# Optimization experiments

Measured on AMD Instinct MI355X. Metric: run time of the kernel, lower is better.

Reference implementation:

```python
import jax, jax.numpy as jnp
import numpy as np
from jax import lax

EPS = 1e-5

# sign binarization with straight-through-estimator gradient (identity),
# matching the .data-swap trick in BinarizeConv2d/BinarizeLinear.
@jax.custom_vjp
def ste_sign(x):
    return jnp.sign(x)

def _ste_fwd(x):
    return jnp.sign(x), None

def _ste_bwd(_, g):
    return (g,)

ste_sign.defvjp(_ste_fwd, _ste_bwd)


def conv3x3(x, w):
    # weight is binarized inside the layer; padding=1, stride=1, no bias
    return lax.conv_general_dilated(
        x, ste_sign(w), window_strides=(1, 1), padding=((1, 1), (1, 1)),
        dimension_numbers=('NCHW', 'OIHW', 'NCHW'))


def mp2(x):
    return lax.reduce_window(x, -jnp.inf, lax.max, (1, 1, 2, 2), (1, 1, 2, 2), 'VALID')


def bn2d(x, gamma, beta):
    # training-mode BatchNorm2d: batch statistics over (N, H, W)
    mu = jnp.mean(x, axis=(0, 2, 3), keepdims=True)
    var = jnp.var(x, axis=(0, 2, 3), keepdims=True)
    xn = (x - mu) * lax.rsqrt(var + EPS)
    return xn * gamma[None, :, None, None] + beta[None, :, None, None]


def bn1d(x, gamma=None, beta=None):
    mu = jnp.mean(x, axis=0, keepdims=True)
    var = jnp.var(x, axis=0, keepdims=True)
    xn = (x - mu) * lax.rsqrt(var + EPS)
    if gamma is None:
        return xn
    return xn * gamma[None, :] + beta[None, :]


def hardtanh(x):
    return jnp.clip(x, -1.0, 1.0)


def setup_inputs() -> dict:
    key = jax.random.key(0)
    ks = jax.random.split(key, 16)
    def w(k, shape):
        return jax.random.normal(k, shape, jnp.float32) * 0.1
    d = {'x': jax.random.normal(ks[0], (512, 3, 32, 32), jnp.float32)}
    convs = [(64, 3), (64, 64), (128, 64), (128, 128), (256, 128), (256, 256)]
    for i, (co, ci) in enumerate(convs):
        d[f'w{i+1}'] = w(ks[1 + i], (co, ci, 3, 3))
        d[f'g{i+1}'] = jnp.ones((co,), jnp.float32)
        d[f'b{i+1}'] = jnp.zeros((co,), jnp.float32)
    d['wf1'] = w(ks[7], (512, 256 * 4 * 4))
    d['gf1'] = jnp.ones((512,), jnp.float32)
    d['bf1'] = jnp.zeros((512,), jnp.float32)
    d['wf2'] = w(ks[8], (512, 512))
    d['gf2'] = jnp.ones((512,), jnp.float32)
    d['bf2'] = jnp.zeros((512,), jnp.float32)
    d['wf3'] = w(ks[9], (10, 512))
    return d


def reference(x, w1, g1, b1, w2, g2, b2, w3, g3, b3, w4, g4, b4,
              w5, g5, b5, w6, g6, b6, wf1, gf1, bf1, wf2, gf2, bf2, wf3):
    # block 1: first conv sees raw 3-channel input (not binarized)
    h = hardtanh(bn2d(conv3x3(x, w1), g1, b1))
    h = hardtanh(bn2d(mp2(conv3x3(ste_sign(h), w2)), g2, b2))
    # block 2
    h = hardtanh(bn2d(conv3x3(ste_sign(h), w3), g3, b3))
    h = hardtanh(bn2d(mp2(conv3x3(ste_sign(h), w4)), g4, b4))
    # block 3
    h = hardtanh(bn2d(conv3x3(ste_sign(h), w5), g5, b5))
    h = hardtanh(bn2d(mp2(conv3x3(ste_sign(h), w6)), g6, b6))
    # classifier (all linear inputs binarized: feature dim != 784)
    h = h.reshape(-1, 256 * 4 * 4)
    h = hardtanh(bn1d(ste_sign(h) @ ste_sign(wf1).T, gf1, bf1))
    h = hardtanh(bn1d(ste_sign(h) @ ste_sign(wf2).T, gf2, bf2))
    h = bn1d(ste_sign(h) @ ste_sign(wf3).T)  # affine=False
    return jax.nn.log_softmax(h, axis=-1)
```

## Files before the change

kernel.cpp:

```cpp
#include <hip/hip_runtime.h>
#include <stdint.h>
#include <math.h>


typedef unsigned long long u64;

__device__ __forceinline__ void flag_and_wave(u64* flag, u64 nz) {
    nz &= __shfl_xor(nz, 1);
    nz &= __shfl_xor(nz, 2);
    nz &= __shfl_xor(nz, 4);
    nz &= __shfl_xor(nz, 8);
    nz &= __shfl_xor(nz, 16);
    nz &= __shfl_xor(nz, 32);
    if ((threadIdx.x & 63) == 0) atomicAnd(flag, nz);
}

__global__ void kflag_init(u64* __restrict__ f) {
    int i = threadIdx.x;
    if (i < 16) f[i] = ~0ull;
}

__global__ void kw1t(const float* __restrict__ w1, float* __restrict__ wt) {
    int i = blockIdx.x * 64 + threadIdx.x;
    if (i >= 64 * 27) return;
    int co = i / 27, k = i % 27;
    float v = w1[i];
    wt[k * 64 + co] = (v > 0.f) ? 1.f : ((v < 0.f) ? -1.f : 0.f);
}

__global__ __launch_bounds__(256) void k1_conv_allv2(const float* __restrict__ x,
                                                     const float* __restrict__ wt,
                                                     float* __restrict__ out) {
    int gid = blockIdx.x * 256 + threadIdx.x;
    int n = gid >> 8, hw0 = (gid & 255) * 4;
    int cbase = blockIdx.y * 32;
    int y = hw0 >> 5, x0 = hw0 & 31;
    const float* ip = x + (size_t)n * 3 * 1024;
    for (int cc = 0; cc < 32; cc += 16) {
        int c0 = cbase + cc;
        float4 a[16];
#pragma unroll
        for (int c = 0; c < 16; ++c) a[c] = make_float4(0.f, 0.f, 0.f, 0.f);
        for (int ky = 0; ky < 3; ++ky) {
            int yy = y + ky - 1;
            bool rowok = (unsigned)yy < 32u;
            float win[3][6];
#pragma unroll
            for (int ci = 0; ci < 3; ++ci)
#pragma unroll
                for (int j = 0; j < 6; ++j) {
                    int ccx = x0 - 1 + j;
                    bool ok = rowok && ((unsigned)ccx < 32u);
                    win[ci][j] = ok ? ip[ci * 1024 + yy * 32 + ccx] : 0.f;
                }
#pragma unroll
            for (int kx = 0; kx < 3; ++kx)
#pragma unroll
                for (int ci = 0; ci < 3; ++ci) {
                    const float* wrow = wt + (ci * 9 + ky * 3 + kx) * 64 + c0;
                    float s0 = win[ci][kx], s1 = win[ci][kx + 1];
                    float s2 = win[ci][kx + 2], s3 = win[ci][kx + 3];
#pragma unroll
                    for (int c = 0; c < 16; ++c) {
                        float wv = wrow[c];
                        a[c].x = fmaf(wv, s0, a[c].x);
                        a[c].y = fmaf(wv, s1, a[c].y);
                        a[c].z = fmaf(wv, s2, a[c].z);
                        a[c].w = fmaf(wv, s3, a[c].w);
                    }
                }
        }
#pragma unroll
        for (int c = 0; c < 16; ++c)
            *(float4*)(out + ((size_t)n * 64 + c0 + c) * 1024 + hw0) = a[c];
    }
}

__global__ void k1_statsA(const float* __restrict__ v, double* __restrict__ Sp,
                          double* __restrict__ S2p, int N) {
    int c = blockIdx.x;
    int slot = blockIdx.y * 64 + threadIdx.x;
    double s = 0.0, s2 = 0.0;
    int K = N * 4;
    const float* vp = v + (size_t)c * 1024 + slot;
    int k0 = 0;
    for (; k0 + 32 <= K; k0 += 32) {
        const float* p0 = vp + (size_t)(k0 >> 2) * 65536;
        float buf[32];
#pragma unroll
        for (int j = 0; j < 32; ++j)
            buf[j] = p0[(size_t)(j >> 2) * 65536 + (j & 3) * 256];
#pragma unroll
        for (int j = 0; j < 32; ++j) {
            double t = (double)buf[j];
            s += t; s2 += t * t;
        }
    }
    for (; k0 < K; ++k0) {
        int m = slot + k0 * 256;
        double t = (double)v[((size_t)(m >> 10) * 64 + c) * 1024 + (m & 1023)];
        s += t; s2 += t * t;
    }
// ... 192 lines not shown
                          const float* __restrict__ w6, const float* __restrict__ wf1,
                          const float* __restrict__ wf2, const float* __restrict__ wf3,
                          u64* wb2B, u64* wb2Z, u64* wb3B, u64* wb3Z,
                          u64* wb4B, u64* wb4Z, u64* wb5B, u64* wb5Z,
                          u64* wb6B, u64* wb6Z, u64* wf1B, u64* wf1Z,
                          u64* wf2B, u64* wf2Z, u64* wf3B, u64* wf3Z,
                          u64* flags) {
    int b = blockIdx.x, t = threadIdx.x;
    if      (b <   3) pack_wconv_body(w2, wb2B, wb2Z,  64,  64, &flags[0], b * 256 + t);
    else if (b <   8) pack_wconv_body(w3, wb3B, wb3Z,  64, 128, &flags[1], (b - 3) * 256 + t);
    else if (b <  17) pack_wconv_body(w4, wb4B, wb4Z, 128, 128, &flags[2], (b - 8) * 256 + t);
    else if (b <  35) pack_wconv_body(w5, wb5B, wb5Z, 128, 256, &flags[3], (b - 17) * 256 + t);
    else if (b <  71) pack_wconv_body(w6, wb6B, wb6Z, 256, 256, &flags[4], (b - 35) * 256 + t);
    else if (b < 199) pack_wlinT_body(wf1, wf1B, wf1Z, 4096, 512, &flags[5], (b - 71) * 256 + t);
    else if (b < 215) pack_wlinT_body(wf2, wf2B, wf2Z,  512, 512, &flags[6], (b - 199) * 256 + t);
    else              pack_wlinT_body(wf3, wf3B, wf3Z,  512,  10, &flags[7], (b - 215) * 256 + t);
}

template <int WRD, int CB>
__device__ __forceinline__ void conv_slow(const u64* __restrict__ ib, const u64* __restrict__ iz,
                                          const u64* __restrict__ wbp, const u64* __restrict__ wzp,
                                          int H, int Wi, int y, int x, int* acc) {
#pragma unroll
    for (int c = 0; c < CB; ++c) acc[c] = 0;
    for (int ky = 0; ky < 3; ++ky) {
        int yy = y + ky - 1;
        if ((unsigned)yy >= (unsigned)H) continue;
        for (int kx = 0; kx < 3; ++kx) {
            int xc = x + kx - 1;
            if ((unsigned)xc >= (unsigned)Wi) continue;
            int p = yy * Wi + xc, t = ky * 3 + kx;
            u64 xb[WRD], xz[WRD];
#pragma unroll
            for (int w = 0; w < WRD; ++w) {
                xb[w] = ib[(size_t)p * WRD + w];
                xz[w] = iz[(size_t)p * WRD + w];
            }
#pragma unroll
            for (int c = 0; c < CB; ++c) {
#pragma unroll
                for (int w = 0; w < WRD; ++w) {
                    u64 e = xz[w] & wzp[(c * 9 + t) * WRD + w];
                    acc[c] += __popcll(e) - 2 * __popcll((xb[w] ^ wbp[(c * 9 + t) * WRD + w]) & e);
                }
            }
        }
    }
}

template <int WRD, int CB>
__device__ __forceinline__ void conv_fast(const u64* __restrict__ ib,
                                          const u64* __restrict__ wbp,
                                          int H, int Wi, int y, int x, int* acc) {
    int a2[CB];
#pragma unroll
    for (int c = 0; c < CB; ++c) a2[c] = 0;
    int T = 0;
    for (int ky = 0; ky < 3; ++ky) {
        int yy = y + ky - 1;
        if ((unsigned)yy >= (unsigned)H) continue;
        for (int kx = 0; kx < 3; ++kx) {
            int xc = x + kx - 1;
            if ((unsigned)xc >= (unsigned)Wi) continue;
            int p = yy * Wi + xc, t = ky * 3 + kx;
            ++T;
            u64 xb[WRD];
#pragma unroll
            for (int w = 0; w < WRD; ++w) xb[w] = ib[(size_t)p * WRD + w];
#pragma unroll
            for (int c = 0; c < CB; ++c)
#pragma unroll
                for (int w = 0; w < WRD; ++w)
                    a2[c] += __popcll(xb[w] ^ wbp[(c * 9 + t) * WRD + w]);
        }
    }
#pragma unroll
    for (int c = 0; c < CB; ++c) acc[c] = 64 * WRD * T - 2 * a2[c];
}

template <int WRD, int CB>
__global__ void kbconv2(const u64* __restrict__ B, const u64* __restrict__ NZ,
                        const u64* __restrict__ WB, const u64* __restrict__ WNZ,
                        int16_t* __restrict__ out, int Co, int H, int Wi,
                        const u64* __restrict__ wflag, const u64* __restrict__ aflag) {
    int hw = blockIdx.x * 64 + threadIdx.x;
    if (hw >= H * Wi) return;
    int co0 = blockIdx.y * CB, n = blockIdx.z;
    int y = hw / Wi, x = hw % Wi;
    const u64* ib = B  + (size_t)n * H * Wi * WRD;
    const u64* iz = NZ + (size_t)n * H * Wi * WRD;
    const u64* wbp = WB  + (size_t)co0 * 9 * WRD;
    const u64* wzp = WNZ + (size_t)co0 * 9 * WRD;
    bool fast = ((*wflag) & (*aflag)) == ~0ull;
    int acc[CB];
    if (fast) conv_fast<WRD, CB>(ib, wbp, H, Wi, y, x, acc);
    else      conv_slow<WRD, CB>(ib, iz, wbp, wzp, H, Wi, y, x, acc);
#pragma unroll
    for (int c = 0; c < CB; ++c)
        out[((size_t)n * Co + co0 + c) * H * Wi + hw] = (int16_t)acc[c];
}

template <int WRD, int CB>
__global__ void kbconv_pool2(const u64* __restrict__ B, const u64* __restrict__ NZ,
                             const u64* __restrict__ WB, const u64* __restrict__ WNZ,
                             int16_t* __restrict__ out, int Co, int H, int Wi,
                             const u64* __restrict__ wflag, const u64* __restrict__ aflag) {
    int Ho = H >> 1, Wo = Wi >> 1;
    int hw = blockIdx.x * 64 + threadIdx.x;
    if (hw >= Ho * Wo) return;
    int co0 = blockIdx.y * CB, n = blockIdx.z;
    int yo = hw / Wo, xo = hw % Wo;
    const u64* ib = B  + (size_t)n * H * Wi * WRD;
    const u64* iz = NZ + (size_t)n * H * Wi * WRD;
    const u64* wbp = WB  + (size_t)co0 * 9 * WRD;
    const u64* wzp = WNZ + (size_t)co0 * 9 * WRD;
    bool fast = ((*wflag) & (*aflag)) == ~0ull;
    int best[CB];
#pragma unroll
    for (int c = 0; c < CB; ++c) best[c] = -(1 << 30);
    if (fast) {
        for (int dy = 0; dy < 2; ++dy)
            for (int dx = 0; dx < 2; ++dx) {
                int acc[CB];
                conv_fast<WRD, CB>(ib, wbp, H, Wi, 2 * yo + dy, 2 * xo + dx, acc);
#pragma unroll
                for (int c = 0; c < CB; ++c) best[c] = acc[c] > best[c] ? acc[c] : best[c];
            }
    } else {
        for (int dy = 0; dy < 2; ++dy)
            for (int dx = 0; dx < 2; ++dx) {
                int acc[CB];
                conv_slow<WRD, CB>(ib, iz, wbp, wzp, H, Wi, 2 * yo + dy, 2 * xo + dx, acc);
#pragma unroll
                for (int c = 0; c < CB; ++c) best[c] = acc[c] > best[c] ? acc[c] : best[c];
            }
    }
#pragma unroll
    for (int c = 0; c < CB; ++c)
        out[((size_t)n * Co + co0 + c) * Ho * Wo + hw] = (int16_t)best[c];
}

template <int WRD, int CB>
__global__ void kbconv_pool2s(const u64* __restrict__ B, const u64* __restrict__ NZ,
                              const u64* __restrict__ WB, const u64* __restrict__ WNZ,
                              int16_t* __restrict__ out, int Co, int H, int Wi,
                              const u64* __restrict__ wflag, const u64* __restrict__ aflag) {
    int Ho = H >> 1, Wo = Wi >> 1;
    int t0 = threadIdx.x;
    int pix = t0 & 15, pos = t0 >> 4;
    int co0 = blockIdx.y * CB, n = blockIdx.z;
    int yo = pix / Wo, xo = pix % Wo;
    int y = 2 * yo + (pos >> 1), x = 2 * xo + (pos & 1);
    const u64* ib = B  + (size_t)n * H * Wi * WRD;
    const u64* iz = NZ + (size_t)n * H * Wi * WRD;
    const u64* wbp = WB  + (size_t)co0 * 9 * WRD;
    const u64* wzp = WNZ + (size_t)co0 * 9 * WRD;
    bool fast = ((*wflag) & (*aflag)) == ~0ull;
    int acc[CB];
    if (fast) conv_fast<WRD, CB>(ib, wbp, H, Wi, y, x, acc);
    else      conv_slow<WRD, CB>(ib, iz, wbp, wzp, H, Wi, y, x, acc);
#pragma unroll
    for (int c = 0; c < CB; ++c) {
        int v = acc[c];
        int v1 = __shfl_xor(v, 16); v = v1 > v ? v1 : v;
        int v2 = __shfl_xor(v, 32); v = v2 > v ? v2 : v;
        acc[c] = v;
    }
    if (pos == 0) {
#pragma unroll
        for (int c = 0; c < CB; ++c)
            out[((size_t)n * Co + co0 + c) * Ho * Wo + pix] = (int16_t)acc[c];
    }
}

__global__ void kaccum16(const int16_t* __restrict__ v, long long* __restrict__ Sp,
                         long long* __restrict__ S2p, int C, int HW, int M) {
    int c = blockIdx.x;
    long long s = 0, s2 = 0;
    int M8 = M >> 3;
    for (int g = blockIdx.y * 256 + threadIdx.x; g < M8; g += gridDim.y * 256) {
        int m0 = g * 8;
        const int16_t* p = v + ((size_t)(m0 / HW) * C + c) * HW + (m0 % HW);
        short4 a = *(const short4*)p;
        short4 b = *(const short4*)(p + 4);
        int v0 = a.x, v1 = a.y, v2 = a.z, v3 = a.w;
        int v4 = b.x, v5 = b.y, v6 = b.z, v7 = b.w;
        s  += v0 + v1 + v2 + v3 + v4 + v5 + v6 + v7;
        s2 += (long long)v0 * v0 + (long long)v1 * v1 + (long long)v2 * v2 + (long long)v3 * v3
            + (long long)v4 * v4 + (long long)v5 * v5 + (long long)v6 * v6 + (long long)v7 * v7;
    }
    __shared__ long long sh[256], sh2[256];
    sh[threadIdx.x] = s; sh2[threadIdx.x] = s2;
    __syncthreads();
    for (int o = 128; o > 0; o >>= 1) {
        if ((int)threadIdx.x < o) { sh[threadIdx.x] += sh[threadIdx.x + o]; sh2[threadIdx.x] += sh2[threadIdx.x + o]; }
        __syncthreads();
    }
    if (threadIdx.x == 0) {
        Sp[c * gridDim.y + blockIdx.y]  = sh[0];
        S2p[c * gridDim.y + blockIdx.y] = sh2[0];
    }
}

__global__ void ksp_conv2(const int16_t* __restrict__ v,
                          const long long* __restrict__ Sp, const long long* __restrict__ S2p,
                          int NB, const float* __restrict__ g, const float* __restrict__ b,
                          u64* __restrict__ B, u64* __restrict__ NZ, int C, int HW, int N,
                          int M, u64* __restrict__ aflag) {
    __shared__ double sMu[256], sA[256], sB[256];
    for (int c = threadIdx.x; c < C; c += 64) {
        long long s = 0, s2 = 0;
        for (int i = 0; i < NB; ++i) { s += Sp[c * NB + i]; s2 += S2p[c * NB + i]; }
        double mean = (double)s / M;
        double var  = (double)s2 / M - mean * mean;
        if (var < 0.0) var = 0.0;
        sMu[c] = mean;
        sA[c]  = (g ? (double)g[c] : 1.0) / sqrt(var + 1e-5);
        sB[c]  = b ? (double)b[c] : 0.0;
    }
    __syncthreads();
    int tid = blockIdx.x * 64 + threadIdx.x;
    int WRD = C >> 6;
    int HW4 = HW >> 2;
    int total = N * WRD * HW4;
    u64 nzall = ~0ull;
    if (tid < total) {
        int hw4 = tid % HW4;
        int wd  = (tid / HW4) % WRD;
        int n   = tid / (HW4 * WRD);
        const int16_t* vp = v + ((size_t)n * C + wd * 64) * HW + hw4 * 4;
        u64 b0 = 0, b1 = 0, b2 = 0, b3 = 0;
        u64 n0 = 0, n1 = 0, n2 = 0, n3 = 0;
        for (int j0 = 0; j0 < 64; j0 += 16) {
            short4 buf[16];
#pragma unroll
            for (int j = 0; j < 16; ++j)
                buf[j] = *(const short4*)(vp + (size_t)(j0 + j) * HW);
#pragma unroll
            for (int j = 0; j < 16; ++j) {
                int c = wd * 64 + j0 + j;
                double Mu = sMu[c], A = sA[c], Bb = sB[c];
                double t0 = ((double)buf[j].x - Mu) * A + Bb;
                double t1 = ((double)buf[j].y - Mu) * A + Bb;
                double t2 = ((double)buf[j].z - Mu) * A + Bb;
                double t3 = ((double)buf[j].w - Mu) * A + Bb;
                int sh = j0 + j;
                b0 |= (u64)(t0 > 0.0) << sh;  n0 |= (u64)(t0 != 0.0) << sh;
                b1 |= (u64)(t1 > 0.0) << sh;  n1 |= (u64)(t1 != 0.0) << sh;
                b2 |= (u64)(t2 > 0.0) << sh;  n2 |= (u64)(t2 != 0.0) << sh;
                b3 |= (u64)(t3 > 0.0) << sh;  n3 |= (u64)(t3 != 0.0) << sh;
            }
        }
        size_t o = ((size_t)n * HW + hw4 * 4) * WRD + wd;
        B[o] = b0;  B[o + WRD] = b1;  B[o + 2 * WRD] = b2;  B[o + 3 * WRD] = b3;
        NZ[o] = n0; NZ[o + WRD] = n1; NZ[o + 2 * WRD] = n2; NZ[o + 3 * WRD] = n3;
        nzall = n0 & n1 & n2 & n3;
    }
    flag_and_wave(aflag, nzall);
}

__global__ void ksp_flat2(const int16_t* __restrict__ v,
                          const long long* __restrict__ Sp, const long long* __restrict__ S2p,
                          int NB, const float* __restrict__ g, const float* __restrict__ b,
                          u64* __restrict__ B, u64* __restrict__ NZ, int M,
                          u64* __restrict__ aflag) {
    __shared__ double sMu[256], sA[256], sB[256];
    for (int c = threadIdx.x; c < 256; c += 64) {
        long long s = 0, s2 = 0;
        for (int i = 0; i < NB; ++i) { s += Sp[c * NB + i]; s2 += S2p[c * NB + i]; }
        double mean = (double)s / M;
        double var  = (double)s2 / M - mean * mean;
        if (var < 0.0) var = 0.0;
        sMu[c] = mean;
        sA[c]  = (g ? (double)g[c] : 1.0) / sqrt(var + 1e-5);
        sB[c]  = b ? (double)b[c] : 0.0;
    }
    __syncthreads();
    int wd = threadIdx.x;
    int n  = blockIdx.x;
    const int16_t* vp = v + (size_t)n * 4096 + wd * 64;
    int16_t buf[64];
#pragma unroll
    for (int j = 0; j < 64; ++j) buf[j] = vp[j];
    u64 b2 = 0, nz = 0;
#pragma unroll
    for (int j = 0; j < 64; ++j) {
        int k = wd * 64 + j;
        int c = k >> 4;
        double t = ((double)buf[j] - sMu[c]) * sA[c] + sB[c];
        b2 |= (u64)(t > 0.0) << j;
        nz |= (u64)(t != 0.0) << j;
    }
    B[(size_t)n * 64 + wd] = b2; NZ[(size_t)n * 64 + wd] = nz;
    flag_and_wave(aflag, nz);
}

__global__ void ksp_fc(const int* __restrict__ v, const double* __restrict__ mu,
                       const double* __restrict__ Ad, const double* __restrict__ Bd,
                       u64* __restrict__ B, u64* __restrict__ NZ, int C, int WRD, int N,
                       u64* __restrict__ aflag) {
    int tid = blockIdx.x * 64 + threadIdx.x;
    u64 nz = ~0ull;
    if (tid < N * WRD) {
        int n = tid / WRD, wd = tid % WRD;
        const int* vp = v + (size_t)n * C + wd * 64;
        int buf[64];
#pragma unroll
        for (int j = 0; j < 64; ++j) buf[j] = vp[j];
        u64 b = 0; nz = 0;
#pragma unroll
        for (int j = 0; j < 64; ++j) {
            int c = wd * 64 + j;
            double t = ((double)buf[j] - mu[c]) * Ad[c] + Bd[c];
            b  |= (u64)(t > 0.0) << j;
            nz |= (u64)(t != 0.0) << j;
        }
        B[(size_t)n * WRD + wd] = b; NZ[(size_t)n * WRD + wd] = nz;
    }
    flag_and_wave(aflag, nz);
}

__global__ void kbfc(const u64* __restrict__ aB, const u64* __restrict__ aNZ,
                     const u64* __restrict__ wBt, const u64* __restrict__ wZt,
                     int* __restrict__ out, int WRD, int O,
                     const u64* __restrict__ wflag, const u64* __restrict__ aflag) {
    int o = blockIdx.x * 64 + threadIdx.x;
    if (o >= O) return;
    int n = blockIdx.y;
    const u64* ab = aB  + (size_t)n * WRD;
    const u64* az = aNZ + (size_t)n * WRD;
    bool fast = ((*wflag) & (*aflag)) == ~0ull;
    int acc;
    if (fast) {
        int a2 = 0;
        for (int w = 0; w < WRD; w += 8) {
            u64 aw[8], ww[8];
#pragma unroll
            for (int j = 0; j < 8; ++j) {
                aw[j] = ab[w + j];
                ww[j] = wBt[(size_t)(w + j) * O + o];
            }
#pragma unroll
            for (int j = 0; j < 8; ++j) a2 += __popcll(aw[j] ^ ww[j]);
        }
        acc = 64 * WRD - 2 * a2;
    } else {
        acc = 0;
        for (int w = 0; w < WRD; ++w) {
            u64 wb = wBt[(size_t)w * O + o];
            u64 wz = wZt[(size_t)w * O + o];
            u64 e = az[w] & wz;
            acc += __popcll(e) - 2 * __popcll((ab[w] ^ wb) & e);
        }
    }
    out[(size_t)n * O + o] = acc;
}

__global__ void k3_stats(const int* __restrict__ v, int N, int C,
                         const float* __restrict__ g, const float* __restrict__ b,
                         double* __restrict__ mu, double* __restrict__ Ad,
                         double* __restrict__ Bd) {
    int c = blockIdx.x;
    __shared__ double sh[256], sh2[256];
    double s = 0.0, s2 = 0.0;
    for (int n = threadIdx.x; n < N; n += 256) {
        double t = (double)v[(size_t)n * C + c];
        s += t; s2 += t * t;
    }
    sh[threadIdx.x] = s; sh2[threadIdx.x] = s2;
    __syncthreads();
    for (int o = 128; o > 0; o >>= 1) {
        if ((int)threadIdx.x < o) { sh[threadIdx.x] += sh[threadIdx.x + o]; sh2[threadIdx.x] += sh2[threadIdx.x + o]; }
        __syncthreads();
    }
    if (threadIdx.x == 0) {
        double mean = sh[0] / N;
        double var  = sh2[0] / N - mean * mean;
        if (var < 0.0) var = 0.0;
        mu[c] = mean;
        Ad[c] = (g ? (double)g[c] : 1.0) / sqrt(var + 1e-5);
        Bd[c] = b ? (double)b[c] : 0.0;
    }
}

__global__ void k4_out(const int* __restrict__ v, const double* __restrict__ mu,
                       const double* __restrict__ Ad, float* __restrict__ out, int N) {
    int n = blockIdx.x * 256 + threadIdx.x;
    if (n >= N) return;
    double z[10];
    double mx = -1e300;
    for (int o = 0; o < 10; ++o) {
        z[o] = ((double)v[n * 10 + o] - mu[o]) * Ad[o];
        if (z[o] > mx) mx = z[o];
    }
    double s = 0.0;
    for (int o = 0; o < 10; ++o) s += exp(z[o] - mx);
    double l = mx + log(s);
    for (int o = 0; o < 10; ++o) out[n * 10 + o] = (float)(z[o] - l);
}

extern "C" void kernel_launch(void* const* d_in, const int* in_sizes, int n_in,
                              void* d_out, int out_size, void* d_ws, size_t ws_size,
                              hipStream_t stream) {
    const int N = in_sizes[0] / (3 * 32 * 32);

    const float* x   = (const float*)d_in[0];
    const float* w1  = (const float*)d_in[1];
    const float* g1  = (const float*)d_in[2];
    const float* b1  = (const float*)d_in[3];
    const float* w2  = (const float*)d_in[4];
    const float* g2  = (const float*)d_in[5];
    const float* b2  = (const float*)d_in[6];
    const float* w3  = (const float*)d_in[7];
    const float* g3  = (const float*)d_in[8];
    const float* b3  = (const float*)d_in[9];
    const float* w4  = (const float*)d_in[10];
    const float* g4  = (const float*)d_in[11];
    const float* b4  = (const float*)d_in[12];
    const float* w5  = (const float*)d_in[13];
    const float* g5  = (const float*)d_in[14];
    const float* b5  = (const float*)d_in[15];
    const float* w6  = (const float*)d_in[16];
    const float* g6  = (const float*)d_in[17];
    const float* b6  = (const float*)d_in[18];
    const float* wf1 = (const float*)d_in[19];
    const float* gf1 = (const float*)d_in[20];
    const float* bf1 = (const float*)d_in[21];
    const float* wf2 = (const float*)d_in[22];
    const float* gf2 = (const float*)d_in[23];
    const float* bf2 = (const float*)d_in[24];
    const float* wf3 = (const float*)d_in[25];

    char* ws = (char*)d_ws;
    size_t off = 0;
    auto alloc = [&](size_t bytes) -> char* {
        char* p = ws + off;
        off = (off + bytes + 511) & ~(size_t)511;
        return p;
    };

    int16_t* t2  = (int16_t*)alloc((size_t)N * 64 * 256 * 2);
    u64* p2B = (u64*)alloc((size_t)N * 256 * 8);
    u64* p2Z = (u64*)alloc((size_t)N * 256 * 8);
    int16_t* t3  = (int16_t*)alloc((size_t)N * 128 * 256 * 2);
    u64* p3B = (u64*)alloc((size_t)N * 256 * 2 * 8);
    u64* p3Z = (u64*)alloc((size_t)N * 256 * 2 * 8);
    int16_t* t4  = (int16_t*)alloc((size_t)N * 128 * 64 * 2);
    u64* p4B = (u64*)alloc((size_t)N * 64 * 2 * 8);
    u64* p4Z = (u64*)alloc((size_t)N * 64 * 2 * 8);
    int16_t* t5  = (int16_t*)alloc((size_t)N * 256 * 64 * 2);
    u64* p5B = (u64*)alloc((size_t)N * 64 * 4 * 8);
    u64* p5Z = (u64*)alloc((size_t)N * 64 * 4 * 8);
    int16_t* t6  = (int16_t*)alloc((size_t)N * 256 * 16 * 2);
    u64* p6B = (u64*)alloc((size_t)N * 64 * 8);
    u64* p6Z = (u64*)alloc((size_t)N * 64 * 8);
    int* fc1 = (int*)alloc((size_t)N * 512 * 4);
    int* fc2 = (int*)alloc((size_t)N * 512 * 4);
    int* fc3 = (int*)alloc((size_t)N * 10 * 4);
    u64* pF1B = (u64*)alloc((size_t)N * 8 * 8);
    u64* pF1Z = (u64*)alloc((size_t)N * 8 * 8);
    u64* pF2B = (u64*)alloc((size_t)N * 8 * 8);
    u64* pF2Z = (u64*)alloc((size_t)N * 8 * 8);
    size_t down_end = off;

    size_t head_big = (size_t)N * 64 * 1024 * 4;
    bool big = ws_size >= head_big + ((size_t)20 << 20);
    float*  c1buf = (float*)ws;
    float*  c1buf8 = (float*)ws;
    int8_t* sgnA  = (int8_t*)(ws + (size_t)N * 8 * 1024 * 4);

    off = big ? (head_big > down_end ? head_big : down_end) : down_end;
    off = (off + 511) & ~(size_t)511;
    u64* p1B = (u64*)alloc((size_t)N * 1024 * 8);
    u64* p1Z = (u64*)alloc((size_t)N * 1024 * 8);
    u64* wb2B = (u64*)alloc(64  * 9 * 1 * 8);  u64* wb2Z = (u64*)alloc(64  * 9 * 1 * 8);
    u64* wb3B = (u64*)alloc(128 * 9 * 1 * 8);  u64* wb3Z = (u64*)alloc(128 * 9 * 1 * 8);
    u64* wb4B = (u64*)alloc(128 * 9 * 2 * 8);  u64* wb4Z = (u64*)alloc(128 * 9 * 2 * 8);
    u64* wb5B = (u64*)alloc(256 * 9 * 2 * 8);  u64* wb5Z = (u64*)alloc(256 * 9 * 2 * 8);
    u64* wb6B = (u64*)alloc(256 * 9 * 4 * 8);  u64* wb6Z = (u64*)alloc(256 * 9 * 4 * 8);
    u64* wf1B = (u64*)alloc(512 * 64 * 8);     u64* wf1Z = (u64*)alloc(512 * 64 * 8);
    u64* wf2B = (u64*)alloc(512 * 8 * 8);      u64* wf2Z = (u64*)alloc(512 * 8 * 8);
    u64* wf3B = (u64*)alloc(10 * 8 * 8);       u64* wf3Z = (u64*)alloc(10 * 8 * 8);
    float* wt = (float*)alloc(27 * 64 * 4);
    double* Sp  = (double*)alloc(64 * 256 * 8);
    double* S2p = (double*)alloc(64 * 256 * 8);
    long long* SpI  = (long long*)alloc(256 * 32 * 8);
    long long* S2pI = (long long*)alloc(256 * 32 * 8);
    u64* flags = (u64*)alloc(16 * 8);
    double* mu = (double*)alloc(512 * 8);
    double* Ad = (double*)alloc(512 * 8);
    double* Bd = (double*)alloc(512 * 8);
    float*  muF = (float*)alloc(64 * 4);
    float*  rF  = (float*)alloc(64 * 4);

    auto cdiv = [](int a, int b) { return (a + b - 1) / b; };

    kflag_init<<<1, 64, 0, stream>>>(flags);
    kpack_all<<<216, 256, 0, stream>>>(w2, w3, w4, w5, w6, wf1, wf2, wf3,
                                       wb2B, wb2Z, wb3B, wb3Z, wb4B, wb4Z,
                                       wb5B, wb5Z, wb6B, wb6Z, wf1B, wf1Z,
                                       wf2B, wf2Z, wf3B, wf3Z, flags);

    if (big) {
        kw1t<<<27, 64, 0, stream>>>(w1, wt);
        k1_conv_allv2<<<dim3((N * 256) / 256, 2), 256, 0, stream>>>(x, wt, c1buf);
        k1_statsA<<<dim3(64, 4), 64, 0, stream>>>(c1buf, Sp, S2p, N);
        k1_statsB<<<64, 256, 0, stream>>>(Sp, S2p, muF, rF, N);
        k1_signpack<<<(N * 256) / 64, 64, 0, stream>>>(c1buf, muF, rF, g1, b1, p1B, p1Z, &flags[8]);
    } else {
        for (int grp = 0; grp < 8; ++grp) {
            k1_conv<<<dim3(16, 8, N), 64, 0, stream>>>(x, w1, c1buf8, grp);
            k1_stats<<<8, 256, 0, stream>>>(c1buf8, muF, rF, grp, N);
            k1_sign<<<dim3(4, 8, N), 256, 0, stream>>>(c1buf8, muF, rF, g1, b1, sgnA, grp);
        }
        kpack_sgn8<<<dim3(16, 1, N), 64, 0, stream>>>(sgnA, p1B, p1Z, 64, 1024, &flags[8]);
    }

    kbconv_pool2<1, 8><<<dim3(4, 8, N), 64, 0, stream>>>(p1B, p1Z, wb2B, wb2Z, t2, 64, 32, 32, &flags[0], &flags[8]);
    kaccum16<<<dim3(64, 32), 256, 0, stream>>>(t2, SpI, S2pI, 64, 256, N * 256);
    ksp_conv2<<<cdiv(N * 1 * 64, 64), 64, 0, stream>>>(t2, SpI, S2pI, 32, g2, b2, p2B, p2Z, 64, 256, N, N * 256, &flags[9]);

    kbconv2<1, 8><<<dim3(4, 16, N), 64, 0, stream>>>(p2B, p2Z, wb3B, wb3Z, t3, 128, 16, 16, &flags[1], &flags[9]);
    kaccum16<<<dim3(128, 16), 256, 0, stream>>>(t3, SpI, S2pI, 128, 256, N * 256);
    ksp_conv2<<<cdiv(N * 2 * 64, 64), 64, 0, stream>>>(t3, SpI, S2pI, 16, g3, b3, p3B, p3Z, 128, 256, N, N * 256, &flags[10]);

    kbconv_pool2<2, 8><<<dim3(1, 16, N), 64, 0, stream>>>(p3B, p3Z, wb4B, wb4Z, t4, 128, 16, 16, &flags[2], &flags[10]);
    kaccum16<<<dim3(128, 16), 256, 0, stream>>>(t4, SpI, S2pI, 128, 64, N * 64);
    ksp_conv2<<<cdiv(N * 2 * 16, 64), 64, 0, stream>>>(t4, SpI, S2pI, 16, g4, b4, p4B, p4Z, 128, 64, N, N * 64, &flags[11]);

    kbconv2<2, 8><<<dim3(1, 32, N), 64, 0, stream>>>(p4B, p4Z, wb5B, wb5Z, t5, 256, 8, 8, &flags[3], &flags[11]);
    kaccum16<<<dim3(256, 8), 256, 0, stream>>>(t5, SpI, S2pI, 256, 64, N * 64);
    ksp_conv2<<<cdiv(N * 4 * 16, 64), 64, 0, stream>>>(t5, SpI, S2pI, 8, g5, b5, p5B, p5Z, 256, 64, N, N * 64, &flags[12]);

    kbconv_pool2s<4, 8><<<dim3(1, 32, N), 64, 0, stream>>>(p5B, p5Z, wb6B, wb6Z, t6, 256, 8, 8, &flags[4], &flags[12]);
    kaccum16<<<dim3(256, 2), 256, 0, stream>>>(t6, SpI, S2pI, 256, 16, N * 16);
    ksp_flat2<<<N, 64, 0, stream>>>(t6, SpI, S2pI, 2, g6, b6, p6B, p6Z, N * 16, &flags[13]);

    kbfc<<<dim3(8, N), 64, 0, stream>>>(p6B, p6Z, wf1B, wf1Z, fc1, 64, 512, &flags[5], &flags[13]);
    k3_stats<<<512, 256, 0, stream>>>(fc1, N, 512, gf1, bf1, mu, Ad, Bd);
    ksp_fc<<<cdiv(N * 8, 64), 64, 0, stream>>>(fc1, mu, Ad, Bd, pF1B, pF1Z, 512, 8, N, &flags[14]);

    kbfc<<<dim3(8, N), 64, 0, stream>>>(pF1B, pF1Z, wf2B, wf2Z, fc2, 8, 512, &flags[6], &flags[14]);
    k3_stats<<<512, 256, 0, stream>>>(fc2, N, 512, gf2, bf2, mu, Ad, Bd);
    ksp_fc<<<cdiv(N * 8, 64), 64, 0, stream>>>(fc2, mu, Ad, Bd, pF2B, pF2Z, 512, 8, N, &flags[15]);

    kbfc<<<dim3(1, N), 64, 0, stream>>>(pF2B, pF2Z, wf3B, wf3Z, fc3, 8, 10, &flags[7], &flags[15]);
    k3_stats<<<10, 256, 0, stream>>>(fc3, N, 10, nullptr, nullptr, mu, Ad, Bd);
    k4_out<<<cdiv(N, 256), 256, 0, stream>>>(fc3, mu, Ad, (float*)d_out, N);
}
```

Before: 648.3 us.

## Fuse batch-norm statistics into conv/fc kernels via bucketed atomics

Each binary conv and fc kernel now reduces per-channel sum and sum-of-squares with wave shuffles and atomically adds them into 16 buckets per channel. This removes the separate kaccum16 and k3_stats passes that re-read the int16/int outputs, and folds the finalisation of mean and variance into the sign-pack and output kernels. A zeroing kernel is added at the start. The cost is atomic contention on the bucket counters, with every fc thread issuing two 64-bit atomics. The final log-softmax now runs in a single block.

```diff
diff --git a/kernel.cpp b/kernel.cpp
--- a/kernel.cpp
+++ b/kernel.cpp
@@ -4,6 +4,9 @@
 
 
 typedef unsigned long long u64;
+
+#define NBK 16
+#define SLOT 8192
 
 __device__ __forceinline__ void flag_and_wave(u64* flag, u64 nz) {
     nz &= __shfl_xor(nz, 1);
@@ -15,9 +18,24 @@
     if ((threadIdx.x & 63) == 0) atomicAnd(flag, nz);
 }
 
-__global__ void kflag_init(u64* __restrict__ f) {
-    int i = threadIdx.x;
-    if (i < 16) f[i] = ~0ull;
+__device__ __forceinline__ void stat_add_wave(long long* Sp, long long* S2p,
+                                              int c, int bucket,
+                                              long long sv, long long s2v) {
+#pragma unroll
+    for (int o = 1; o < 64; o <<= 1) {
+        sv  += __shfl_xor(sv, o);
+        s2v += __shfl_xor(s2v, o);
+    }
+    if ((threadIdx.x & 63) == 0) {
+        atomicAdd((u64*)&Sp[c * NBK + bucket],  (u64)sv);
+        atomicAdd((u64*)&S2p[c * NBK + bucket], (u64)s2v);
+    }
+}
+
+__global__ void kinit(u64* __restrict__ f, long long* __restrict__ SALL, int n) {
+    int i = blockIdx.x * 256 + threadIdx.x;
+    if (i < n) SALL[i] = 0;
+    if (blockIdx.x == 0 && threadIdx.x < 16) f[threadIdx.x] = ~0ull;
 }
 
 __global__ void kw1t(const float* __restrict__ w1, float* __restrict__ wt) {
@@ -376,69 +394,92 @@
 __global__ void kbconv2(const u64* __restrict__ B, const u64* __restrict__ NZ,
                         const u64* __restrict__ WB, const u64* __restrict__ WNZ,
                         int16_t* __restrict__ out, int Co, int H, int Wi,
-                        const u64* __restrict__ wflag, const u64* __restrict__ aflag) {
+                        const u64* __restrict__ wflag, const u64* __restrict__ aflag,
+                        long long* __restrict__ Sp, long long* __restrict__ S2p) {
     int hw = blockIdx.x * 64 + threadIdx.x;
-    if (hw >= H * Wi) return;
+    bool act = hw < H * Wi;
     int co0 = blockIdx.y * CB, n = blockIdx.z;
-    int y = hw / Wi, x = hw % Wi;
-    const u64* ib = B  + (size_t)n * H * Wi * WRD;
-    const u64* iz = NZ + (size_t)n * H * Wi * WRD;
-    const u64* wbp = WB  + (size_t)co0 * 9 * WRD;
-    const u64* wzp = WNZ + (size_t)co0 * 9 * WRD;
-    bool fast = ((*wflag) & (*aflag)) == ~0ull;
     int acc[CB];
-    if (fast) conv_fast<WRD, CB>(ib, wbp, H, Wi, y, x, acc);
-    else      conv_slow<WRD, CB>(ib, iz, wbp, wzp, H, Wi, y, x, acc);
-#pragma unroll
-    for (int c = 0; c < CB; ++c)
-        out[((size_t)n * Co + co0 + c) * H * Wi + hw] = (int16_t)acc[c];
+#pragma unroll
+    for (int c = 0; c < CB; ++c) acc[c] = 0;
+    if (act) {
+        int y = hw / Wi, x = hw % Wi;
+        const u64* ib = B  + (size_t)n * H * Wi * WRD;
+        const u64* iz = NZ + (size_t)n * H * Wi * WRD;
+        const u64* wbp = WB  + (size_t)co0 * 9 * WRD;
+        const u64* wzp = WNZ + (size_t)co0 * 9 * WRD;
+        bool fast = ((*wflag) & (*aflag)) == ~0ull;
+        if (fast) conv_fast<WRD, CB>(ib, wbp, H, Wi, y, x, acc);
+        else      conv_slow<WRD, CB>(ib, iz, wbp, wzp, H, Wi, y, x, acc);
+#pragma unroll
+        for (int c = 0; c < CB; ++c)
+            out[((size_t)n * Co + co0 + c) * H * Wi + hw] = (int16_t)acc[c];
+    }
+    int bucket = blockIdx.z & (NBK - 1);
+#pragma unroll
+    for (int c = 0; c < CB; ++c) {
+        long long v = act ? acc[c] : 0;
+        stat_add_wave(Sp, S2p, co0 + c, bucket, v, v * v);
+    }
 }
 
 template <int WRD, int CB>
 __global__ void kbconv_pool2(const u64* __restrict__ B, const u64* __restrict__ NZ,
                              const u64* __restrict__ WB, const u64* __restrict__ WNZ,
                              int16_t* __restrict__ out, int Co, int H, int Wi,
-                             const u64* __restrict__ wflag, const u64* __restrict__ aflag) {
+                             const u64* __restrict__ wflag, const u64* __restrict__ aflag,
+                             long long* __restrict__ Sp, long long* __restrict__ S2p) {
     int Ho = H >> 1, Wo = Wi >> 1;
     int hw = blockIdx.x * 64 + threadIdx.x;
-    if (hw >= Ho * Wo) return;
+    bool act = hw < Ho * Wo;
     int co0 = blockIdx.y * CB, n = blockIdx.z;
-    int yo = hw / Wo, xo = hw % Wo;
-    const u64* ib = B  + (size_t)n * H * Wi * WRD;
-    const u64* iz = NZ + (size_t)n * H * Wi * WRD;
-    const u64* wbp = WB  + (size_t)co0 * 9 * WRD;
-    const u64* wzp = WNZ + (size_t)co0 * 9 * WRD;
-    bool fast = ((*wflag) & (*aflag)) == ~0ull;
     int best[CB];
 #pragma unroll
-    for (int c = 0; c < CB; ++c) best[c] = -(1 << 30);
-    if (fast) {
-        for (int dy = 0; dy < 2; ++dy)
-            for (int dx = 0; dx < 2; ++dx) {
-                int acc[CB];
-                conv_fast<WRD, CB>(ib, wbp, H, Wi, 2 * yo + dy, 2 * xo + dx, acc);
-#pragma unroll
-                for (int c = 0; c < CB; ++c) best[c] = acc[c] > best[c] ? acc[c] : best[c];
-            }
-    } else {
-        for (int dy = 0; dy < 2; ++dy)
-            for (int dx = 0; dx < 2; ++dx) {
-                int acc[CB];
-                conv_slow<WRD, CB>(ib, iz, wbp, wzp, H, Wi, 2 * yo + dy, 2 * xo + dx, acc);
-#pragma unroll
-                for (int c = 0; c < CB; ++c) best[c] = acc[c] > best[c] ? acc[c] : best[c];
-            }
-    }
-#pragma unroll
-    for (int c = 0; c < CB; ++c)
-        out[((size_t)n * Co + co0 + c) * Ho * Wo + hw] = (int16_t)best[c];
+    for (int c = 0; c < CB; ++c) best[c] = 0;
+    if (act) {
+        int yo = hw / Wo, xo = hw % Wo;
+        const u64* ib = B  + (size_t)n * H * Wi * WRD;
+        const u64* iz = NZ + (size_t)n * H * Wi * WRD;
+        const u64* wbp = WB  + (size_t)co0 * 9 * WRD;
+        const u64* wzp = WNZ + (size_t)co0 * 9 * WRD;
+        bool fast = ((*wflag) & (*aflag)) == ~0ull;
+#pragma unroll
+        for (int c = 0; c < CB; ++c) best[c] = -(1 << 30);
+        if (fast) {
+            for (int dy = 0; dy < 2; ++dy)
+                for (int dx = 0; dx < 2; ++dx) {
+                    int acc[CB];
+                    conv_fast<WRD, CB>(ib, wbp, H, Wi, 2 * yo + dy, 2 * xo + dx, acc);
+#pragma unroll
+                    for (int c = 0; c < CB; ++c) best[c] = acc[c] > best[c] ? acc[c] : best[c];
+                }
+        } else {
+            for (int dy = 0; dy < 2; ++dy)
+                for (int dx = 0; dx < 2; ++dx) {
+                    int acc[CB];
+                    conv_slow<WRD, CB>(ib, iz, wbp, wzp, H, Wi, 2 * yo + dy, 2 * xo + dx, acc);
+#pragma unroll
+                    for (int c = 0; c < CB; ++c) best[c] = acc[c] > best[c] ? acc[c] : best[c];
+                }
+        }
+#pragma unroll
+        for (int c = 0; c < CB; ++c)
+            out[((size_t)n * Co + co0 + c) * Ho * Wo + hw] = (int16_t)best[c];
+    }
+    int bucket = blockIdx.z & (NBK - 1);
+#pragma unroll
+    for (int c = 0; c < CB; ++c) {
+        long long v = act ? best[c] : 0;
+        stat_add_wave(Sp, S2p, co0 + c, bucket, v, v * v);
+    }
 }
 
 template <int WRD, int CB>
 __global__ void kbconv_pool2s(const u64* __restrict__ B, const u64* __restrict__ NZ,
                               const u64* __restrict__ WB, const u64* __restrict__ WNZ,
                               int16_t* __restrict__ out, int Co, int H, int Wi,
-                              const u64* __restrict__ wflag, const u64* __restrict__ aflag) {
+                              const u64* __restrict__ wflag, const u64* __restrict__ aflag,
+                              long long* __restrict__ Sp, long long* __restrict__ S2p) {
     int Ho = H >> 1, Wo = Wi >> 1;
     int t0 = threadIdx.x;
     int pix = t0 & 15, pos = t0 >> 4;
@@ -465,46 +506,23 @@
         for (int c = 0; c < CB; ++c)
             out[((size_t)n * Co + co0 + c) * Ho * Wo + pix] = (int16_t)acc[c];
     }
-}
-
-__global__ void kaccum16(const int16_t* __restrict__ v, long long* __restrict__ Sp,
-                         long long* __restrict__ S2p, int C, int HW, int M) {
-    int c = blockIdx.x;
-    long long s = 0, s2 = 0;
-    int M8 = M >> 3;
-    for (int g = blockIdx.y * 256 + threadIdx.x; g < M8; g += gridDim.y * 256) {
-        int m0 = g * 8;
-        const int16_t* p = v + ((size_t)(m0 / HW) * C + c) * HW + (m0 % HW);
-        short4 a = *(const short4*)p;
-        short4 b = *(const short4*)(p + 4);
-        int v0 = a.x, v1 = a.y, v2 = a.z, v3 = a.w;
-        int v4 = b.x, v5 = b.y, v6 = b.z, v7 = b.w;
-        s  += v0 + v1 + v2 + v3 + v4 + v5 + v6 + v7;
-        s2 += (long long)v0 * v0 + (long long)v1 * v1 + (long long)v2 * v2 + (long long)v3 * v3
-            + (long long)v4 * v4 + (long long)v5 * v5 + (long long)v6 * v6 + (long long)v7 * v7;
-    }
-    __shared__ long long sh[256], sh2[256];
-    sh[threadIdx.x] = s; sh2[threadIdx.x] = s2;
-    __syncthreads();
-    for (int o = 128; o > 0; o >>= 1) {
-        if ((int)threadIdx.x < o) { sh[threadIdx.x] += sh[threadIdx.x + o]; sh2[threadIdx.x] += sh2[threadIdx.x + o]; }
-        __syncthreads();
-    }
-    if (threadIdx.x == 0) {
-        Sp[c * gridDim.y + blockIdx.y]  = sh[0];
-        S2p[c * gridDim.y + blockIdx.y] = sh2[0];
+    int bucket = blockIdx.z & (NBK - 1);
+#pragma unroll
+    for (int c = 0; c < CB; ++c) {
+        long long v = (pos == 0) ? acc[c] : 0;
+        stat_add_wave(Sp, S2p, co0 + c, bucket, v, v * v);
     }
 }
 
 __global__ void ksp_conv2(const int16_t* __restrict__ v,
                           const long long* __restrict__ Sp, const long long* __restrict__ S2p,
-                          int NB, const float* __restrict__ g, const float* __restrict__ b,
+                          const float* __restrict__ g, const float* __restrict__ b,
                           u64* __restrict__ B, u64* __restrict__ NZ, int C, int HW, int N,
                           int M, u64* __restrict__ aflag) {
     __shared__ double sMu[256], sA[256], sB[256];
     for (int c = threadIdx.x; c < C; c += 64) {
         long long s = 0, s2 = 0;
-        for (int i = 0; i < NB; ++i) { s += Sp[c * NB + i]; s2 += S2p[c * NB + i]; }
+        for (int i = 0; i < NBK; ++i) { s += Sp[c * NBK + i]; s2 += S2p[c * NBK + i]; }
         double mean = (double)s / M;
         double var  = (double)s2 / M - mean * mean;
         if (var < 0.0) var = 0.0;
@@ -555,13 +573,13 @@
 
 __global__ void ksp_flat2(const int16_t* __restrict__ v,
                           const long long* __restrict__ Sp, const long long* __restrict__ S2p,
-                          int NB, const float* __restrict__ g, const float* __restrict__ b,
+                          const float* __restrict__ g, const float* __restrict__ b,
                           u64* __restrict__ B, u64* __restrict__ NZ, int M,
                           u64* __restrict__ aflag) {
     __shared__ double sMu[256], sA[256], sB[256];
     for (int c = threadIdx.x; c < 256; c += 64) {
         long long s = 0, s2 = 0;
-        for (int i = 0; i < NB; ++i) { s += Sp[c * NB + i]; s2 += S2p[c * NB + i]; }
+        for (int i = 0; i < NBK; ++i) { s += Sp[c * NBK + i]; s2 += S2p[c * NBK + i]; }
         double mean = (double)s / M;
         double var  = (double)s2 / M - mean * mean;
         if (var < 0.0) var = 0.0;
@@ -589,10 +607,23 @@
     flag_and_wave(aflag, nz);
 }
 
-__global__ void ksp_fc(const int* __restrict__ v, const double* __restrict__ mu,
-                       const double* __restrict__ Ad, const double* __restrict__ Bd,
-                       u64* __restrict__ B, u64* __restrict__ NZ, int C, int WRD, int N,
-                       u64* __restrict__ aflag) {
+__global__ void ksp_fc2(const int* __restrict__ v,
+                        const long long* __restrict__ Sp, const long long* __restrict__ S2p,
+                        const float* __restrict__ g, const float* __restrict__ b,
+                        u64* __restrict__ B, u64* __restrict__ NZ, int C, int WRD, int N,
+                        u64* __restrict__ aflag) {
+    __shared__ double sMu[512], sA[512], sB[512];
+    for (int c = threadIdx.x; c < C; c += 64) {
+        long long s = 0, s2 = 0;
+        for (int i = 0; i < NBK; ++i) { s += Sp[c * NBK + i]; s2 += S2p[c * NBK + i]; }
+        double mean = (double)s / N;
+        double var  = (double)s2 / N - mean * mean;
+        if (var < 0.0) var = 0.0;
+        sMu[c] = mean;
+        sA[c]  = (g ? (double)g[c] : 1.0) / sqrt(var + 1e-5);
+        sB[c]  = b ? (double)b[c] : 0.0;
+    }
+    __syncthreads();
     int tid = blockIdx.x * 64 + threadIdx.x;
     u64 nz = ~0ull;
     if (tid < N * WRD) {
@@ -601,15 +632,15 @@
         int buf[64];
 #pragma unroll
         for (int j = 0; j < 64; ++j) buf[j] = vp[j];
-        u64 b = 0; nz = 0;
+        u64 b2 = 0; nz = 0;
 #pragma unroll
         for (int j = 0; j < 64; ++j) {
             int c = wd * 64 + j;
-            double t = ((double)buf[j] - mu[c]) * Ad[c] + Bd[c];
-            b  |= (u64)(t > 0.0) << j;
+            double t = ((double)buf[j] - sMu[c]) * sA[c] + sB[c];
+            b2 |= (u64)(t > 0.0) << j;
             nz |= (u64)(t != 0.0) << j;
         }
-        B[(size_t)n * WRD + wd] = b; NZ[(size_t)n * WRD + wd] = nz;
+        B[(size_t)n * WRD + wd] = b2; NZ[(size_t)n * WRD + wd] = nz;
     }
     flag_and_wave(aflag, nz);
 }
@@ -617,7 +648,8 @@
 __global__ void kbfc(const u64* __restrict__ aB, const u64* __restrict__ aNZ,
                      const u64* __restrict__ wBt, const u64* __restrict__ wZt,
                      int* __restrict__ out, int WRD, int O,
-                     const u64* __restrict__ wflag, const u64* __restrict__ aflag) {
+                     const u64* __restrict__ wflag, const u64* __restrict__ aflag,
+                     long long* __restrict__ Sp, long long* __restrict__ S2p) {
     int o = blockIdx.x * 64 + threadIdx.x;
     if (o >= O) return;
     int n = blockIdx.y;
@@ -648,49 +680,38 @@
         }
     }
     out[(size_t)n * O + o] = acc;
-}
-
-__global__ void k3_stats(const int* __restrict__ v, int N, int C,
-                         const float* __restrict__ g, const float* __restrict__ b,
-                         double* __restrict__ mu, double* __restrict__ Ad,
-                         double* __restrict__ Bd) {
-    int c = blockIdx.x;
-    __shared__ double sh[256], sh2[256];
-    double s = 0.0, s2 = 0.0;
+    int bucket = n & (NBK - 1);
+    atomicAdd((u64*)&Sp[o * NBK + bucket],  (u64)(long long)acc);
+    atomicAdd((u64*)&S2p[o * NBK + bucket], (u64)((long long)acc * acc));
+}
+
+__global__ void k4_out2(const int* __restrict__ v,
+                        const long long* __restrict__ Sp, const long long* __restrict__ S2p,
+                        float* __restrict__ out, int N) {
+    __shared__ double sMu[10], sA[10];
+    if (threadIdx.x < 10) {
+        int c = threadIdx.x;
+        long long s = 0, s2 = 0;
+        for (int i = 0; i < NBK; ++i) { s += Sp[c * NBK + i]; s2 += S2p[c * NBK + i]; }
+        double mean = (double)s / N;
+        double var  = (double)s2 / N - mean * mean;
+        if (var < 0.0) var = 0.0;
+        sMu[c] = mean;
+        sA[c]  = 1.0 / sqrt(var + 1e-5);
+    }
+    __syncthreads();
     for (int n = threadIdx.x; n < N; n += 256) {
-        double t = (double)v[(size_t)n * C + c];
-        s += t; s2 += t * t;
-    }
-    sh[threadIdx.x] = s; sh2[threadIdx.x] = s2;
-    __syncthreads();
-    for (int o = 128; o > 0; o >>= 1) {
-        if ((int)threadIdx.x < o) { sh[threadIdx.x] += sh[threadIdx.x + o]; sh2[threadIdx.x] += sh2[threadIdx.x + o]; }
-        __syncthreads();
-    }
-    if (threadIdx.x == 0) {
-        double mean = sh[0] / N;
-        double var  = sh2[0] / N - mean * mean;
-        if (var < 0.0) var = 0.0;
-        mu[c] = mean;
-        Ad[c] = (g ? (double)g[c] : 1.0) / sqrt(var + 1e-5);
-        Bd[c] = b ? (double)b[c] : 0.0;
-    }
-}
-
-__global__ void k4_out(const int* __restrict__ v, const double* __restrict__ mu,
-                       const double* __restrict__ Ad, float* __restrict__ out, int N) {
-    int n = blockIdx.x * 256 + threadIdx.x;
-    if (n >= N) return;
-    double z[10];
-    double mx = -1e300;
-    for (int o = 0; o < 10; ++o) {
-        z[o] = ((double)v[n * 10 + o] - mu[o]) * Ad[o];
-        if (z[o] > mx) mx = z[o];
-    }
-    double s = 0.0;
-    for (int o = 0; o < 10; ++o) s += exp(z[o] - mx);
-    double l = mx + log(s);
-    for (int o = 0; o < 10; ++o) out[n * 10 + o] = (float)(z[o] - l);
+        double z[10];
+        double mx = -1e300;
+        for (int o = 0; o < 10; ++o) {
+            z[o] = ((double)v[n * 10 + o] - sMu[o]) * sA[o];
+            if (z[o] > mx) mx = z[o];
+        }
+        double s = 0.0;
+        for (int o = 0; o < 10; ++o) s += exp(z[o] - mx);
+        double l = mx + log(s);
+        for (int o = 0; o < 10; ++o) out[n * 10 + o] = (float)(z[o] - l);
+    }
 }
 
 extern "C" void kernel_launch(void* const* d_in, const int* in_sizes, int n_in,
@@ -758,7 +779,7 @@
     size_t down_end = off;
 
     size_t head_big = (size_t)N * 64 * 1024 * 4;
-    bool big = ws_size >= head_big + ((size_t)20 << 20);
+    bool big = ws_size >= head_big + ((size_t)24 << 20);
     float*  c1buf = (float*)ws;
     float*  c1buf8 = (float*)ws;
     int8_t* sgnA  = (int8_t*)(ws + (size_t)N * 8 * 1024 * 4);
@@ -778,18 +799,17 @@
     float* wt = (float*)alloc(27 * 64 * 4);
     double* Sp  = (double*)alloc(64 * 256 * 8);
     double* S2p = (double*)alloc(64 * 256 * 8);
-    long long* SpI  = (long long*)alloc(256 * 32 * 8);
-    long long* S2pI = (long long*)alloc(256 * 32 * 8);
+    long long* SALL = (long long*)alloc((size_t)8 * 2 * SLOT * 8);
     u64* flags = (u64*)alloc(16 * 8);
-    double* mu = (double*)alloc(512 * 8);
-    double* Ad = (double*)alloc(512 * 8);
-    double* Bd = (double*)alloc(512 * 8);
     float*  muF = (float*)alloc(64 * 4);
     float*  rF  = (float*)alloc(64 * 4);
 
+    auto SPs  = [&](int s) { return SALL + (size_t)s * 2 * SLOT; };
+    auto S2Ps = [&](int s) { return SALL + (size_t)s * 2 * SLOT + SLOT; };
+
     auto cdiv = [](int a, int b) { return (a + b - 1) / b; };
 
-    kflag_init<<<1, 64, 0, stream>>>(flags);
+    kinit<<<cdiv(8 * 2 * SLOT, 256), 256, 0, stream>>>(flags, SALL, 8 * 2 * SLOT);
     kpack_all<<<216, 256, 0, stream>>>(w2, w3, w4, w5, w6, wf1, wf2, wf3,
                                        wb2B, wb2Z, wb3B, wb3Z, wb4B, wb4Z,
                                        wb5B, wb5Z, wb6B, wb6Z, wf1B, wf1Z,
@@ -810,35 +830,27 @@
         kpack_sgn8<<<dim3(16, 1, N), 64, 0, stream>>>(sgnA, p1B, p1Z, 64, 1024, &flags[8]);
     }
 
-    kbconv_pool2<1, 8><<<dim3(4, 8, N), 64, 0, stream>>>(p1B, p1Z, wb2B, wb2Z, t2, 64, 32, 32, &flags[0], &flags[8]);
-    kaccum16<<<dim3(64, 32), 256, 0, stream>>>(t2, SpI, S2pI, 64, 256, N * 256);
-    ksp_conv2<<<cdiv(N * 1 * 64, 64), 64, 0, stream>>>(t2, SpI, S2pI, 32, g2, b2, p2B, p2Z, 64, 256, N, N * 256, &flags[9]);
-
-    kbconv2<1, 8><<<dim3(4, 16, N), 64, 0, stream>>>(p2B, p2Z, wb3B, wb3Z, t3, 128, 16, 16, &flags[1], &flags[9]);
-    kaccum16<<<dim3(128, 16), 256, 0, stream>>>(t3, SpI, S2pI, 128, 256, N * 256);
-    ksp_conv2<<<cdiv(N * 2 * 64, 64), 64, 0, stream>>>(t3, SpI, S2pI, 16, g3, b3, p3B, p3Z, 128, 256, N, N * 256, &flags[10]);
-
-    kbconv_pool2<2, 8><<<dim3(1, 16, N), 64, 0, stream>>>(p3B, p3Z, wb4B, wb4Z, t4, 128, 16, 16, &flags[2], &flags[10]);
-    kaccum16<<<dim3(128, 16), 256, 0, stream>>>(t4, SpI, S2pI, 128, 64, N * 64);
-    ksp_conv2<<<cdiv(N * 2 * 16, 64), 64, 0, stream>>>(t4, SpI, S2pI, 16, g4, b4, p4B, p4Z, 128, 64, N, N * 64, &flags[11]);
-
-    kbconv2<2, 8><<<dim3(1, 32, N), 64, 0, stream>>>(p4B, p4Z, wb5B, wb5Z, t5, 256, 8, 8, &flags[3], &flags[11]);
-    kaccum16<<<dim3(256, 8), 256, 0, stream>>>(t5, SpI, S2pI, 256, 64, N * 64);
-    ksp_conv2<<<cdiv(N * 4 * 16, 64), 64, 0, stream>>>(t5, SpI, S2pI, 8, g5, b5, p5B, p5Z, 256, 64, N, N * 64, &flags[12]);
-
-    kbconv_pool2s<4, 8><<<dim3(1, 32, N), 64, 0, stream>>>(p5B, p5Z, wb6B, wb6Z, t6, 256, 8, 8, &flags[4], &flags[12]);
-    kaccum16<<<dim3(256, 2), 256, 0, stream>>>(t6, SpI, S2pI, 256, 16, N * 16);
-    ksp_flat2<<<N, 64, 0, stream>>>(t6, SpI, S2pI, 2, g6, b6, p6B, p6Z, N * 16, &flags[13]);
-
-    kbfc<<<dim3(8, N), 64, 0, stream>>>(p6B, p6Z, wf1B, wf1Z, fc1, 64, 512, &flags[5], &flags[13]);
-    k3_stats<<<512, 256, 0, stream>>>(fc1, N, 512, gf1, bf1, mu, Ad, Bd);
-    ksp_fc<<<cdiv(N * 8, 64), 64, 0, stream>>>(fc1, mu, Ad, Bd, pF1B, pF1Z, 512, 8, N, &flags[14]);
-
-    kbfc<<<dim3(8, N), 64, 0, stream>>>(pF1B, pF1Z, wf2B, wf2Z, fc2, 8, 512, &flags[6], &flags[14]);
-    k3_stats<<<512, 256, 0, stream>>>(fc2, N, 512, gf2, bf2, mu, Ad, Bd);
-    ksp_fc<<<cdiv(N * 8, 64), 64, 0, stream>>>(fc2, mu, Ad, Bd, pF2B, pF2Z, 512, 8, N, &flags[15]);
-
-    kbfc<<<dim3(1, N), 64, 0, stream>>>(pF2B, pF2Z, wf3B, wf3Z, fc3, 8, 10, &flags[7], &flags[15]);
-    k3_stats<<<10, 256, 0, stream>>>(fc3, N, 10, nullptr, nullptr, mu, Ad, Bd);
-    k4_out<<<cdiv(N, 256), 256, 0, stream>>>(fc3, mu, Ad, (float*)d_out, N);
-}
+    kbconv_pool2<1, 8><<<dim3(4, 8, N), 64, 0, stream>>>(p1B, p1Z, wb2B, wb2Z, t2, 64, 32, 32, &flags[0], &flags[8], SPs(0), S2Ps(0));
+    ksp_conv2<<<cdiv(N * 1 * 64, 64), 64, 0, stream>>>(t2, SPs(0), S2Ps(0), g2, b2, p2B, p2Z, 64, 256, N, N * 256, &flags[9]);
+
+    kbconv2<1, 8><<<dim3(4, 16, N), 64, 0, stream>>>(p2B, p2Z, wb3B, wb3Z, t3, 128, 16, 16, &flags[1], &flags[9], SPs(1), S2Ps(1));
+    ksp_conv2<<<cdiv(N * 2 * 64, 64), 64, 0, stream>>>(t3, SPs(1), S2Ps(1), g3, b3, p3B, p3Z, 128, 256, N, N * 256, &flags[10]);
+
+    kbconv_pool2<2, 8><<<dim3(1, 16, N), 64, 0, stream>>>(p3B, p3Z, wb4B, wb4Z, t4, 128, 16, 16, &flags[2], &flags[10], SPs(2), S2Ps(2));
+    ksp_conv2<<<cdiv(N * 2 * 16, 64), 64, 0, stream>>>(t4, SPs(2), S2Ps(2), g4, b4, p4B, p4Z, 128, 64, N, N * 64, &flags[11]);
+
+    kbconv2<2, 8><<<dim3(1, 32, N), 64, 0, stream>>>(p4B, p4Z, wb5B, wb5Z, t5, 256, 8, 8, &flags[3], &flags[11], SPs(3), S2Ps(3));
+    ksp_conv2<<<cdiv(N * 4 * 16, 64), 64, 0, stream>>>(t5, SPs(3), S2Ps(3), g5, b5, p5B, p5Z, 256, 64, N, N * 64, &flags[12]);
+
+    kbconv_pool2s<4, 8><<<dim3(1, 32, N), 64, 0, stream>>>(p5B, p5Z, wb6B, wb6Z, t6, 256, 8, 8, &flags[4], &flags[12], SPs(4), S2Ps(4));
+    ksp_flat2<<<N, 64, 0, stream>>>(t6, SPs(4), S2Ps(4), g6, b6, p6B, p6Z, N * 16, &flags[13]);
+
+    kbfc<<<dim3(8, N), 64, 0, stream>>>(p6B, p6Z, wf1B, wf1Z, fc1, 64, 512, &flags[5], &flags[13], SPs(5), S2Ps(5));
+    ksp_fc2<<<cdiv(N * 8, 64), 64, 0, stream>>>(fc1, SPs(5), S2Ps(5), gf1, bf1, pF1B, pF1Z, 512, 8, N, &flags[14]);
+
+    kbfc<<<dim3(8, N), 64, 0, stream>>>(pF1B, pF1Z, wf2B, wf2Z, fc2, 8, 512, &flags[6], &flags[14], SPs(6), S2Ps(6));
+    ksp_fc2<<<cdiv(N * 8, 64), 64, 0, stream>>>(fc2, SPs(6), S2Ps(6), gf2, bf2, pF2B, pF2Z, 512, 8, N, &flags[15]);
+
+    kbfc<<<dim3(1, N), 64, 0, stream>>>(pF2B, pF2Z, wf3B, wf3Z, fc3, 8, 10, &flags[7], &flags[15], SPs(7), S2Ps(7));
+    k4_out2<<<1, 256, 0, stream>>>(fc3, SPs(7), S2Ps(7), (float*)d_out, N);
+}
```

Result: slower. 777.2 us (+19.9%).
